# Kernel optimization log

Measured on AMD Instinct MI355X. Metric: run time of the kernel, lower is better.

Reference implementation:

```python
import jax, jax.numpy as jnp
import numpy as np

HEADS = 8
KV_HEADS = 4
HEAD_DIM = 256
HIDDEN = 2560
WINDOW = 1024          # sliding_window (layer is sliding: (0+1) % 6 != 0)
SCALE = 256.0 ** -0.5  # query_pre_attn_scalar ** -0.5
ROPE_BASE = 10000.0    # rope_local_base_freq for sliding layers
EPS = 1e-6
NEG = -1e30


def rms_norm(x, w, eps=EPS):
    # x: [..., D]; effective weight is (1 + param) per the RMSNorm module
    var = jnp.mean(x * x, axis=-1, keepdims=True)
    return x * jax.lax.rsqrt(var + eps) * w


def rope(x, base, offset):
    # x: [B, H, T, D]; rotate-half RoPE over the full head_dim
    T, D = x.shape[2], x.shape[3]
    half = D // 2
    pos = (offset + jnp.arange(T)).astype(jnp.float32)           # [T]
    inv_freq = base ** (-jnp.arange(half, dtype=jnp.float32) * 2.0 / D)  # [half]
    ang = pos[:, None] * inv_freq[None, :]                       # [T, half]
    cos, sin = jnp.cos(ang), jnp.sin(ang)
    x1, x2 = x[..., :half], x[..., half:]
    return jnp.concatenate([x1 * cos - x2 * sin, x2 * cos + x1 * sin], axis=-1)


def setup_inputs() -> dict:
    key = jax.random.key(0)
    ks = jax.random.split(key, 7)
    B, T, S = 2, 1024, 4096
    w_std = 0.02
    return {
        "x": jax.random.normal(ks[0], (B, T, HIDDEN), dtype=jnp.float32),
        "k_cache": jax.random.normal(ks[1], (B, KV_HEADS, S, HEAD_DIM), dtype=jnp.float32),
        "v_cache": jax.random.normal(ks[2], (B, KV_HEADS, S, HEAD_DIM), dtype=jnp.float32),
        "wq": jax.random.normal(ks[3], (HIDDEN, HEADS * HEAD_DIM), dtype=jnp.float32) * w_std,
        "wk": jax.random.normal(ks[4], (HIDDEN, KV_HEADS * HEAD_DIM), dtype=jnp.float32) * w_std,
        "wv": jax.random.normal(ks[5], (HIDDEN, KV_HEADS * HEAD_DIM), dtype=jnp.float32) * w_std,
        "wo": jax.random.normal(ks[6], (HEADS * HEAD_DIM, HIDDEN), dtype=jnp.float32) * w_std,
        "q_norm_w": jnp.zeros((HEAD_DIM,), dtype=jnp.float32),
        "k_norm_w": jnp.zeros((HEAD_DIM,), dtype=jnp.float32),
        "pos_offset": 2048,
        "cache_index": 2048,
    }


def reference(x, k_cache, v_cache, wq, wk, wv, wo, q_norm_w, k_norm_w, pos_offset, cache_index):
    B, T, _ = x.shape
    # QKV projections -> [B, H, T, D]
    q = (x @ wq).reshape(B, T, HEADS, HEAD_DIM).transpose(0, 2, 1, 3)
    k = (x @ wk).reshape(B, T, KV_HEADS, HEAD_DIM).transpose(0, 2, 1, 3)
    v = (x @ wv).reshape(B, T, KV_HEADS, HEAD_DIM).transpose(0, 2, 1, 3)
    # per-head RMSNorm (effective weight 1 + param)
    q = rms_norm(q, 1.0 + q_norm_w)
    k = rms_norm(k, 1.0 + k_norm_w)
    # RoPE with position offset
    q = rope(q, ROPE_BASE, pos_offset)
    k = rope(k, ROPE_BASE, pos_offset)
    # KV cache update at cache_index along the sequence axis
    k_new = jax.lax.dynamic_update_slice(k_cache, k, (0, 0, cache_index, 0))
    v_new = jax.lax.dynamic_update_slice(v_cache, v, (0, 0, cache_index, 0))
    S = k_new.shape[2]
    # sliding-window validity mask over cached keys (as in the module: shared over queries)
    idx = jnp.arange(S)
    valid = (idx < cache_index + T) & (idx >= cache_index + T - WINDOW)   # [S]
    # GQA attention: group queries over kv heads
    G = HEADS // KV_HEADS
    qg = q.reshape(B, KV_HEADS, G, T, HEAD_DIM)
    scores = jnp.einsum('bkgtd,bksd->bkgts', qg, k_new) * SCALE           # [B,KV,G,T,S]
    scores = jnp.where(valid[None, None, None, None, :], scores, NEG)
    p = jax.nn.softmax(scores, axis=-1)
    out = jnp.einsum('bkgts,bksd->bkgtd', p, v_new)                       # [B,KV,G,T,D]
    out = out.reshape(B, HEADS, T, HEAD_DIM).transpose(0, 2, 1, 3).reshape(B, T, HEADS * HEAD_DIM)
    return out @ wo, k_new, v_new
```

## Files before the change

### kernel.cpp

```cpp
#include <hip/hip_runtime.h>

typedef __bf16 bf16;
typedef __bf16 bf16x8 __attribute__((ext_vector_type(8)));
typedef __bf16 bf16x4 __attribute__((ext_vector_type(4)));
typedef float f32x4 __attribute__((ext_vector_type(4)));

#define MFMA16(a, b, c) __builtin_amdgcn_mfma_f32_16x16x32_bf16(a, b, c, 0, 0, 0)

#define GLL(lds, g)                                                    \
  __builtin_amdgcn_global_load_lds(                                    \
      (const __attribute__((address_space(1))) void*)(g),              \
      (__attribute__((address_space(3))) void*)(lds), 16, 0, 0)

__global__ __launch_bounds__(256) void cvt_x_kernel(const float* __restrict__ x,
                                                    bf16* __restrict__ xb) {
  const long i = (long)blockIdx.x * 256 + threadIdx.x;
  const float4 v = ((const float4*)x)[i];
  bf16x4 o4;
  o4.x = (bf16)v.x; o4.y = (bf16)v.y; o4.z = (bf16)v.z; o4.w = (bf16)v.w;
  ((bf16x4*)xb)[i] = o4;
}

__global__ __launch_bounds__(256) void wqkv_trans_kernel(const float* __restrict__ wq,
                                                         const float* __restrict__ wk,
                                                         const float* __restrict__ wv,
                                                         bf16* __restrict__ dst) {
  __shared__ float tile[32][33];
  const int k0 = blockIdx.x * 32, n0 = blockIdx.y * 32;
  const float* src; int col, srcN;
  if (n0 < 2048)      { src = wq; col = n0;        srcN = 2048; }
  else if (n0 < 3072) { src = wk; col = n0 - 2048; srcN = 1024; }
  else                { src = wv; col = n0 - 3072; srcN = 1024; }
  const int tx = threadIdx.x, ty = threadIdx.y;
#pragma unroll
  for (int i = 0; i < 4; ++i)
    tile[ty + i * 8][tx] = src[(long)(k0 + ty + i * 8) * srcN + col + tx];
  __syncthreads();
#pragma unroll
  for (int i = 0; i < 4; ++i)
    dst[(long)(n0 + ty + i * 8) * 2560 + k0 + tx] = (bf16)tile[tx][ty + i * 8];
}

__global__ __launch_bounds__(256) void wo_trans_kernel(const float* __restrict__ wo,
                                                       bf16* __restrict__ dst) {
  __shared__ float tile[32][33];
  const int k0 = blockIdx.x * 32, n0 = blockIdx.y * 32;
  const int tx = threadIdx.x, ty = threadIdx.y;
#pragma unroll
  for (int i = 0; i < 4; ++i)
    tile[ty + i * 8][tx] = wo[(long)(k0 + ty + i * 8) * 2560 + n0 + tx];
  __syncthreads();
#pragma unroll
  for (int i = 0; i < 4; ++i)
    dst[(long)(n0 + ty + i * 8) * 2048 + k0 + tx] = (bf16)tile[tx][ty + i * 8];
}

__global__ __launch_bounds__(256) void v_trans_kernel(const float* __restrict__ vout,
                                                      const int* __restrict__ p_ci,
                                                      bf16* __restrict__ vt) {
  __shared__ float tile[32][33];
  const int s0 = blockIdx.x * 32, d0 = blockIdx.y * 32, bk = blockIdx.z;
  const int ci = *p_ci;
  const int tx = threadIdx.x, ty = threadIdx.y;
  const float* src = vout + ((long)bk * 4096 + ci) * 256;
#pragma unroll
  for (int i = 0; i < 4; ++i)
    tile[ty + i * 8][tx] = src[(long)(s0 + ty + i * 8) * 256 + d0 + tx];
  __syncthreads();
  bf16* dstb = vt + ((long)bk * 256 + d0) * 1024 + s0;
#pragma unroll
  for (int i = 0; i < 4; ++i)
    dstb[(long)(ty + i * 8) * 1024 + tx] = (bf16)tile[tx][ty + i * 8];
}

template <int K, int N>
__global__ __launch_bounds__(256) void gemm_kernel(const bf16* __restrict__ A,
                                                   const bf16* __restrict__ BT,
                                                   float* __restrict__ C) {
  __shared__ bf16 As[128 * 32];
  __shared__ bf16 Bs[128 * 32];
  const int bm = blockIdx.x, bn = blockIdx.y;
  const int tid = threadIdx.x;
  const int wave = tid >> 6, lane = tid & 63;
  const int quad = lane >> 4, l16 = lane & 15;
  const int wm = (wave & 1) * 64, wn = (wave >> 1) * 64;
  f32x4 acc[4][4] = {};
  const int r0 = tid >> 2;
  const int cc0 = ((tid & 3) - (r0 >> 1)) & 3;
  const int r1 = r0 + 64;
  const int cc1 = ((tid & 3) - (r1 >> 1)) & 3;
  const bf16* Ag = A + (long)(bm * 128) * K;
  const bf16* Bg = BT + (long)(bn * 128) * K;
  bf16* AsW  = As + wave * 512;
  bf16* AsW2 = As + 2048 + wave * 512;
  bf16* BsW  = Bs + wave * 512;
  bf16* BsW2 = Bs + 2048 + wave * 512;
  for (int k0 = 0; k0 < K; k0 += 32) {
    __syncthreads();
    GLL(AsW, Ag + (long)r0 * K + k0 + cc0 * 8);
    GLL(AsW2, Ag + (long)r1 * K + k0 + cc1 * 8);
    GLL(BsW, Bg + (long)r0 * K + k0 + cc0 * 8);
    GLL(BsW2, Bg + (long)r1 * K + k0 + cc1 * 8);
    __syncthreads();
    bf16x8 af[4], bfr[4];
#pragma unroll
    for (int mi = 0; mi < 4; ++mi) {
      const int r = wm + mi * 16 + l16;
      af[mi] = *(const bf16x8*)(As + r * 32 + (((quad + (r >> 1)) & 3) * 8));
    }
#pragma unroll
    for (int ni = 0; ni < 4; ++ni) {
      const int r = wn + ni * 16 + l16;
      bfr[ni] = *(const bf16x8*)(Bs + r * 32 + (((quad + (r >> 1)) & 3) * 8));
    }
#pragma unroll
    for (int mi = 0; mi < 4; ++mi)
#pragma unroll
      for (int ni = 0; ni < 4; ++ni)
        acc[mi][ni] = MFMA16(af[mi], bfr[ni], acc[mi][ni]);
  }
  const int crow = bm * 128 + wm + quad * 4;
  const int ccol = bn * 128 + wn + l16;
#pragma unroll
  for (int mi = 0; mi < 4; ++mi)
#pragma unroll
    for (int ni = 0; ni < 4; ++ni)
#pragma unroll
      for (int r = 0; r < 4; ++r)
        C[(long)(crow + mi * 16 + r) * N + ccol + ni * 16] = acc[mi][ni][r];
}

__global__ __launch_bounds__(256) void normrope_kernel(
    const float* __restrict__ qkv, const float* __restrict__ qw,
    const float* __restrict__ kw, const int* __restrict__ p_pos,
    const int* __restrict__ p_ci, float* __restrict__ kout,
    float* __restrict__ vout, bf16* __restrict__ q_bf, bf16* __restrict__ k_bf) {
  const int bt = blockIdx.x, slot = blockIdx.y;
  const int t = bt & 1023, b = bt >> 10;
  const int d = threadIdx.x;
  const float val = qkv[(long)bt * 4096 + slot * 256 + d];
  const int ci = *p_ci;
  if (slot >= 12) {
    vout[((long)(b * 4 + (slot - 12)) * 4096 + ci + t) * 256 + d] = val;
    return;
  }
  __shared__ float red[4];
  __shared__ float rowbuf[256];
  float ss = val * val;
#pragma unroll
  for (int i = 1; i < 64; i <<= 1) ss += __shfl_xor(ss, i);
  if ((d & 63) == 0) red[d >> 6] = ss;
  __syncthreads();
  const float tot = red[0] + red[1] + red[2] + red[3];
  const float rstd = rsqrtf(tot * (1.0f / 256.0f) + 1e-6f);
  const bool isq = slot < 8;
  const float wv = isq ? qw[d] : kw[d];
  const float nv = val * rstd * (1.0f + wv);
  rowbuf[d] = nv;
  __syncthreads();
  const int e = d & 127;
  const float inv_freq = exp2f((float)e * -0.10381025296522976f);
  const float ang = (float)(*p_pos + t) * inv_freq;
  float sn, cs;
  sincosf(ang, &sn, &cs);
  float outv;
  if (d < 128) outv = nv * cs - rowbuf[d + 128] * sn;
  else         outv = nv * cs + rowbuf[d - 128] * sn;
  if (isq) {
    q_bf[((long)(b * 8 + slot) * 1024 + t) * 256 + d] = (bf16)outv;
  } else {
    const int kh = slot - 8;
    kout[((long)(b * 4 + kh) * 4096 + ci + t) * 256 + d] = outv;
    k_bf[((long)(b * 4 + kh) * 1024 + t) * 256 + d] = (bf16)outv;
  }
}

__global__ __launch_bounds__(256) void attn_kernel(const bf16* __restrict__ q_bf,
                                                   const bf16* __restrict__ k_bf,
                                                   const bf16* __restrict__ vt_bf,
                                                   bf16* __restrict__ attn) {
  __shared__ bf16 Ks[64 * 256];
  __shared__ bf16 Vs[256 * 64];
  __shared__ bf16 Ps[64 * 72];
  const int qt = blockIdx.x, h = blockIdx.y, b = blockIdx.z;
  const int kvh = h >> 1;
  const int tid = threadIdx.x;
  const int wave = tid >> 6, lane = tid & 63, quad = lane >> 4, l16 = lane & 15;
  bf16x8 qf[8];
  const bf16* qg =
      q_bf + ((long)(b * 8 + h) * 1024 + qt * 64 + wave * 16 + l16) * 256 + quad * 8;
#pragma unroll
  for (int i = 0; i < 8; ++i) qf[i] = *(const bf16x8*)(qg + i * 32);
  f32x4 o[16] = {};
  float m_r[4] = {-1e30f, -1e30f, -1e30f, -1e30f};
  float l_r[4] = {0.f, 0.f, 0.f, 0.f};
  const float sfac = 0.0625f * 1.44269504088896f;
  const bf16* kgb = k_bf + (long)(b * 4 + kvh) * 1024 * 256;
  const bf16* vgb = vt_bf + (long)(b * 4 + kvh) * 256 * 1024;
  const int krow = tid >> 5, kccp = tid & 31;
  const int kcc = kccp ^ (krow & 7);
  const int vrow0 = tid >> 3, vccp = tid & 7;
  for (int st = 0; st < 16; ++st) {
    __syncthreads();
#pragma unroll
    for (int i = 0; i < 8; ++i) {
      GLL(Ks + (i * 256 + wave * 64) * 8,
          kgb + (long)(st * 64 + krow + i * 8) * 256 + kcc * 8);
    }
#pragma unroll
    for (int i = 0; i < 8; ++i) {
      const int vr = vrow0 + i * 32;
      GLL(Vs + (i * 256 + wave * 64) * 8,
          vgb + (long)vr * 1024 + st * 64 + (vccp ^ (vr & 7)) * 8);
    }
    __syncthreads();
    f32x4 sacc[4] = {};
#pragma unroll
    for (int kk = 0; kk < 8; ++kk) {
#pragma unroll
      for (int ni = 0; ni < 4; ++ni) {
        const int r = ni * 16 + l16;
        bf16x8 kf = *(const bf16x8*)(Ks + r * 256 + (((kk * 4 + quad) ^ (r & 7)) * 8));
        sacc[ni] = MFMA16(qf[kk], kf, sacc[ni]);
      }
    }
    float alpha_r[4];
#pragma unroll
    for (int r = 0; r < 4; ++r) {
      float s0 = sacc[0][r] * sfac, s1 = sacc[1][r] * sfac;
      float s2 = sacc[2][r] * sfac, s3 = sacc[3][r] * sfac;
      float mx = fmaxf(fmaxf(s0, s1), fmaxf(s2, s3));
#pragma unroll
      for (int dd = 1; dd < 16; dd <<= 1) mx = fmaxf(mx, __shfl_xor(mx, dd));
      float mnew = fmaxf(m_r[r], mx);
      float al = exp2f(m_r[r] - mnew);
      m_r[r] = mnew;
      alpha_r[r] = al;
      float p0 = exp2f(s0 - mnew), p1 = exp2f(s1 - mnew);
      float p2 = exp2f(s2 - mnew), p3 = exp2f(s3 - mnew);
      float rs = p0 + p1 + p2 + p3;
#pragma unroll
      for (int dd = 1; dd < 16; dd <<= 1) rs += __shfl_xor(rs, dd);
      l_r[r] = l_r[r] * al + rs;
      const int prow = (wave * 16 + quad * 4 + r) * 72;
      Ps[prow + l16] = (bf16)p0;
      Ps[prow + 16 + l16] = (bf16)p1;
      Ps[prow + 32 + l16] = (bf16)p2;
      Ps[prow + 48 + l16] = (bf16)p3;
    }
#pragma unroll
    for (int n2 = 0; n2 < 16; ++n2) {
      f32x4 tv = o[n2];
      tv.x *= alpha_r[0]; tv.y *= alpha_r[1]; tv.z *= alpha_r[2]; tv.w *= alpha_r[3];
      o[n2] = tv;
    }
    __syncthreads();
    bf16x8 pf0 = *(const bf16x8*)(Ps + (wave * 16 + l16) * 72 + quad * 8);
    bf16x8 pf1 = *(const bf16x8*)(Ps + (wave * 16 + l16) * 72 + 32 + quad * 8);
#pragma unroll
    for (int n2 = 0; n2 < 16; ++n2) {
      const int r = n2 * 16 + l16;
      bf16x8 vf0 = *(const bf16x8*)(Vs + r * 64 + ((quad ^ (r & 7)) * 8));
      o[n2] = MFMA16(pf0, vf0, o[n2]);
      bf16x8 vf1 = *(const bf16x8*)(Vs + r * 64 + (((4 + quad) ^ (r & 7)) * 8));
      o[n2] = MFMA16(pf1, vf1, o[n2]);
    }
  }
  float inv_l[4];
#pragma unroll
  for (int r = 0; r < 4; ++r) inv_l[r] = 1.0f / l_r[r];
  bf16* og = attn + ((long)(b * 1024 + qt * 64 + wave * 16 + quad * 4)) * 2048 +
             h * 256 + l16;
#pragma unroll
  for (int n2 = 0; n2 < 16; ++n2)
#pragma unroll
    for (int r = 0; r < 4; ++r)
      og[(long)r * 2048 + n2 * 16] = (bf16)(o[n2][r] * inv_l[r]);
}

extern "C" void kernel_launch(void* const* d_in, const int* in_sizes, int n_in,
                              void* d_out, int out_size, void* d_ws, size_t ws_size,
                              hipStream_t stream) {
  const float* x = (const float*)d_in[0];
  const float* k_cache = (const float*)d_in[1];
  const float* v_cache = (const float*)d_in[2];
  const float* wq = (const float*)d_in[3];
  const float* wk = (const float*)d_in[4];
  const float* wv = (const float*)d_in[5];
  const float* wo = (const float*)d_in[6];
  const float* qnw = (const float*)d_in[7];
  const float* knw = (const float*)d_in[8];
  const int* p_pos = (const int*)d_in[9];
  const int* p_ci = (const int*)d_in[10];

  float* out0 = (float*)d_out;
  float* kout = out0 + (long)2 * 1024 * 2560;
  float* vout = kout + (long)2 * 4 * 4096 * 256;

  char* w = (char*)d_ws;
  bf16* x_bf = (bf16*)(w);
  bf16* wqkv_t = (bf16*)(w + 10485760);
  bf16* wo_t = (bf16*)(w + 31457280);
  float* qkv = (float*)(w + 41943040);
  bf16* q_bf = (bf16*)(w + 75497472);
  bf16* k_bf = (bf16*)(w + 83886080);
  bf16* vt_bf = (bf16*)(w + 88080384);
  bf16* attn_b = (bf16*)(w + 92274688);

  hipMemcpyAsync(kout, k_cache, (size_t)8388608 * 4, hipMemcpyDeviceToDevice, stream);
  hipMemcpyAsync(vout, v_cache, (size_t)8388608 * 4, hipMemcpyDeviceToDevice, stream);

  cvt_x_kernel<<<5120, 256, 0, stream>>>(x, x_bf);
  dim3 tb(32, 8);
  wqkv_trans_kernel<<<dim3(80, 128), tb, 0, stream>>>(wq, wk, wv, wqkv_t);
  wo_trans_kernel<<<dim3(64, 80), tb, 0, stream>>>(wo, wo_t);

  gemm_kernel<2560, 4096><<<dim3(16, 32), 256, 0, stream>>>(x_bf, wqkv_t, qkv);

  normrope_kernel<<<dim3(2048, 16), 256, 0, stream>>>(qkv, qnw, knw, p_pos, p_ci,
                                                      kout, vout, q_bf, k_bf);

  v_trans_kernel<<<dim3(32, 8, 8), tb, 0, stream>>>(vout, p_ci, vt_bf);

  attn_kernel<<<dim3(16, 8, 2), 256, 0, stream>>>(q_bf, k_bf, vt_bf, attn_b);

  gemm_kernel<2048, 2560><<<dim3(16, 20), 256, 0, stream>>>(attn_b, wo_t, out0);
}
```

Baseline: 420.6 us.

## Skip overwritten cache rows in copy kernel and retile GEMM to 128x64x64

Replaces the two full device-to-device memcpys of the KV caches with a kernel that copies everything except the 1024 rows normrope will overwrite, avoiding redundant writes. The GEMM tile changes from 128x128 with K-step 32 to 128x64 with K-step 64 and an XOR swizzle, doubling the grid so more blocks fill the CUs and halving barrier count per K. The trade-off is lower per-block reuse of A and a custom copy kernel that may reach lower bandwidth than the runtime memcpy.

```diff
diff --git a/kernel.cpp b/kernel.cpp
--- a/kernel.cpp
+++ b/kernel.cpp
@@ -11,6 +11,19 @@
   __builtin_amdgcn_global_load_lds(                                    \
       (const __attribute__((address_space(1))) void*)(g),              \
       (__attribute__((address_space(3))) void*)(lds), 16, 0, 0)
+
+__global__ __launch_bounds__(256) void cache_copy_kernel(
+    const float* __restrict__ kc, const float* __restrict__ vc,
+    float* __restrict__ kout, float* __restrict__ vout,
+    const int* __restrict__ p_ci) {
+  const int s = blockIdx.x * 4 + (threadIdx.x >> 6);
+  const int bk = blockIdx.y;
+  const int ci = *p_ci;
+  if ((unsigned)(s - ci) < 1024u) return;
+  const long base = ((long)bk * 4096 + s) * 64 + (threadIdx.x & 63);
+  ((float4*)kout)[base] = ((const float4*)kc)[base];
+  ((float4*)vout)[base] = ((const float4*)vc)[base];
+}
 
 __global__ __launch_bounds__(256) void cvt_x_kernel(const float* __restrict__ x,
                                                     bf16* __restrict__ xb) {
@@ -77,54 +90,57 @@
 __global__ __launch_bounds__(256) void gemm_kernel(const bf16* __restrict__ A,
                                                    const bf16* __restrict__ BT,
                                                    float* __restrict__ C) {
-  __shared__ bf16 As[128 * 32];
-  __shared__ bf16 Bs[128 * 32];
+  __shared__ bf16 As[128 * 64];
+  __shared__ bf16 Bs[64 * 64];
   const int bm = blockIdx.x, bn = blockIdx.y;
   const int tid = threadIdx.x;
   const int wave = tid >> 6, lane = tid & 63;
   const int quad = lane >> 4, l16 = lane & 15;
-  const int wm = (wave & 1) * 64, wn = (wave >> 1) * 64;
-  f32x4 acc[4][4] = {};
-  const int r0 = tid >> 2;
-  const int cc0 = ((tid & 3) - (r0 >> 1)) & 3;
-  const int r1 = r0 + 64;
-  const int cc1 = ((tid & 3) - (r1 >> 1)) & 3;
+  const int wm = (wave & 1) * 64, wn = (wave >> 1) * 32;
+  f32x4 acc[4][2] = {};
+  const int srow = tid >> 3;
+  const int scol = tid & 7;
   const bf16* Ag = A + (long)(bm * 128) * K;
-  const bf16* Bg = BT + (long)(bn * 128) * K;
-  bf16* AsW  = As + wave * 512;
-  bf16* AsW2 = As + 2048 + wave * 512;
-  bf16* BsW  = Bs + wave * 512;
-  bf16* BsW2 = Bs + 2048 + wave * 512;
-  for (int k0 = 0; k0 < K; k0 += 32) {
-    __syncthreads();
-    GLL(AsW, Ag + (long)r0 * K + k0 + cc0 * 8);
-    GLL(AsW2, Ag + (long)r1 * K + k0 + cc1 * 8);
-    GLL(BsW, Bg + (long)r0 * K + k0 + cc0 * 8);
-    GLL(BsW2, Bg + (long)r1 * K + k0 + cc1 * 8);
-    __syncthreads();
-    bf16x8 af[4], bfr[4];
-#pragma unroll
-    for (int mi = 0; mi < 4; ++mi) {
-      const int r = wm + mi * 16 + l16;
-      af[mi] = *(const bf16x8*)(As + r * 32 + (((quad + (r >> 1)) & 3) * 8));
-    }
-#pragma unroll
-    for (int ni = 0; ni < 4; ++ni) {
-      const int r = wn + ni * 16 + l16;
-      bfr[ni] = *(const bf16x8*)(Bs + r * 32 + (((quad + (r >> 1)) & 3) * 8));
-    }
-#pragma unroll
-    for (int mi = 0; mi < 4; ++mi)
-#pragma unroll
-      for (int ni = 0; ni < 4; ++ni)
-        acc[mi][ni] = MFMA16(af[mi], bfr[ni], acc[mi][ni]);
+  const bf16* Bg = BT + (long)(bn * 64) * K;
+  for (int k0 = 0; k0 < K; k0 += 64) {
+    __syncthreads();
+#pragma unroll
+    for (int i = 0; i < 4; ++i) {
+      const int r = i * 32 + srow;
+      GLL(As + (i * 256 + wave * 64) * 8, Ag + (long)r * K + k0 + (scol ^ (r & 7)) * 8);
+    }
+#pragma unroll
+    for (int i = 0; i < 2; ++i) {
+      const int r = i * 32 + srow;
+      GLL(Bs + (i * 256 + wave * 64) * 8, Bg + (long)r * K + k0 + (scol ^ (r & 7)) * 8);
+    }
+    __syncthreads();
+#pragma unroll
+    for (int kk = 0; kk < 2; ++kk) {
+      bf16x8 af[4], bfr[2];
+#pragma unroll
+      for (int mi = 0; mi < 4; ++mi) {
+        const int r = wm + mi * 16 + l16;
+        af[mi] = *(const bf16x8*)(As + r * 64 + (((kk * 4 + quad) ^ (r & 7)) * 8));
+      }
+#pragma unroll
+      for (int ni = 0; ni < 2; ++ni) {
+        const int r = wn + ni * 16 + l16;
+        bfr[ni] = *(const bf16x8*)(Bs + r * 64 + (((kk * 4 + quad) ^ (r & 7)) * 8));
+      }
+#pragma unroll
+      for (int mi = 0; mi < 4; ++mi)
+#pragma unroll
+        for (int ni = 0; ni < 2; ++ni)
+          acc[mi][ni] = MFMA16(af[mi], bfr[ni], acc[mi][ni]);
+    }
   }
   const int crow = bm * 128 + wm + quad * 4;
-  const int ccol = bn * 128 + wn + l16;
+  const int ccol = bn * 64 + wn + l16;
 #pragma unroll
   for (int mi = 0; mi < 4; ++mi)
 #pragma unroll
-    for (int ni = 0; ni < 4; ++ni)
+    for (int ni = 0; ni < 2; ++ni)
 #pragma unroll
       for (int r = 0; r < 4; ++r)
         C[(long)(crow + mi * 16 + r) * N + ccol + ni * 16] = acc[mi][ni][r];
@@ -307,15 +323,15 @@
   bf16* vt_bf = (bf16*)(w + 88080384);
   bf16* attn_b = (bf16*)(w + 92274688);
 
-  hipMemcpyAsync(kout, k_cache, (size_t)8388608 * 4, hipMemcpyDeviceToDevice, stream);
-  hipMemcpyAsync(vout, v_cache, (size_t)8388608 * 4, hipMemcpyDeviceToDevice, stream);
+  cache_copy_kernel<<<dim3(1024, 8), 256, 0, stream>>>(k_cache, v_cache, kout,
+                                                       vout, p_ci);
 
   cvt_x_kernel<<<5120, 256, 0, stream>>>(x, x_bf);
   dim3 tb(32, 8);
   wqkv_trans_kernel<<<dim3(80, 128), tb, 0, stream>>>(wq, wk, wv, wqkv_t);
   wo_trans_kernel<<<dim3(64, 80), tb, 0, stream>>>(wo, wo_t);
 
-  gemm_kernel<2560, 4096><<<dim3(16, 32), 256, 0, stream>>>(x_bf, wqkv_t, qkv);
+  gemm_kernel<2560, 4096><<<dim3(16, 64), 256, 0, stream>>>(x_bf, wqkv_t, qkv);
 
   normrope_kernel<<<dim3(2048, 16), 256, 0, stream>>>(qkv, qnw, knw, p_pos, p_ci,
                                                       kout, vout, q_bf, k_bf);
@@ -324,5 +340,5 @@
 
   attn_kernel<<<dim3(16, 8, 2), 256, 0, stream>>>(q_bf, k_bf, vt_bf, attn_b);
 
-  gemm_kernel<2048, 2560><<<dim3(16, 20), 256, 0, stream>>>(attn_b, wo_t, out0);
-}
+  gemm_kernel<2048, 2560><<<dim3(16, 40), 256, 0, stream>>>(attn_b, wo_t, out0);
+}
```

Measured after the change: 395.5 us. 6.0% less time.
